# Optimization experiments

Hardware: AMD Instinct MI355X
Metric: run time of the kernel (lower is better)

The kernel has to match this reference:

```python
import jax, jax.numpy as jnp
import numpy as np

B, S, IN, OUT = 4, 2048, 4096, 11008


def setup_inputs() -> dict:
    key = jax.random.key(0)
    k1, k2, k3, k4 = jax.random.split(key, 4)
    x = jax.random.normal(k1, (B, S, IN), dtype=jnp.float32)
    # int8 weight codes (stored as int32 for portability; values in [0,127))
    weight_int8 = jax.random.randint(k2, (OUT, IN), 0, 127, dtype=jnp.int32)
    scale = jax.random.uniform(k3, (OUT,), dtype=jnp.float32) * 0.01 + 1e-4
    bias = jax.random.normal(k4, (OUT,), dtype=jnp.float32)
    return {"x": x, "weight_int8": weight_int8, "scale": scale, "bias": bias}


def reference(x, weight_int8, scale, bias):
    # dequantize: int8 codes -> fp, per-output-row scale (scale.view(-1,1) in torch)
    w = weight_int8.astype(jnp.float32) * scale[:, None]  # [OUT, IN]
    # F.linear(x, w, bias) == x @ w.T + bias
    out = jnp.einsum('bsi,oi->bso', x, w) + bias  # [B, S, OUT]
    return out
```

## Files before the change

kernel.cpp:

```cpp
#include <hip/hip_runtime.h>
#include <hip/hip_bf16.h>
#include <stdint.h>


#define MT 8192
#define KT 4096
#define NT 11008
#define NKT 32
#define MTILES 32
#define NTILES 43
#define CHUNK_BYTES 32768

typedef __attribute__((ext_vector_type(8))) short short8;
typedef __attribute__((ext_vector_type(4))) float f32x4;
typedef __attribute__((ext_vector_type(4))) int i32x4;
typedef __attribute__((ext_vector_type(16))) char char16;

static __device__ __forceinline__ short f2bf(float f) {
  union { float f; unsigned u; } c; c.f = f;
  unsigned u = c.u;
  return (short)((u + 0x7fffu + ((u >> 16) & 1u)) >> 16);
}

__global__ __launch_bounds__(256) void quant_x_kernel(const float* __restrict__ in,
                                                      char* __restrict__ Aws,
                                                      float* __restrict__ sx) {
  const int m = blockIdx.x;
  const int t = threadIdx.x;
  const float* row = in + (size_t)m * KT + t * 16;
  f32x4 v[4];
  float mx = 0.f;
#pragma unroll
  for (int i = 0; i < 4; i++) {
    v[i] = *(const f32x4*)(row + i * 4);
#pragma unroll
    for (int j = 0; j < 4; j++) mx = fmaxf(mx, fabsf(v[i][j]));
  }
#pragma unroll
  for (int off = 32; off; off >>= 1) mx = fmaxf(mx, __shfl_xor(mx, off));
  __shared__ float smx[4];
  if ((t & 63) == 0) smx[t >> 6] = mx;
  __syncthreads();
  mx = fmaxf(fmaxf(smx[0], smx[1]), fmaxf(smx[2], smx[3]));
  const float inv = 127.0f / mx;
  if (t == 0) sx[m] = mx * (1.0f / 127.0f);
  char16 q;
#pragma unroll
  for (int i = 0; i < 4; i++)
#pragma unroll
    for (int j = 0; j < 4; j++) q[i * 4 + j] = (char)(int)rintf(v[i][j] * inv);
  const int mt = m >> 8, r = m & 255, kt = t >> 3, g = t & 7;
  *(char16*)(Aws + ((size_t)mt * NKT + kt) * CHUNK_BYTES + r * 128 +
             ((g * 16) ^ ((r & 7) << 4))) = q;
}

__global__ __launch_bounds__(256) void cvt_w8_kernel(const int* __restrict__ in,
                                                     char* __restrict__ Bws) {
  const int n = blockIdx.x;
  const int t = threadIdx.x;
  const int* s = in + (size_t)n * KT + t * 16;
  char16 q;
#pragma unroll
  for (int i = 0; i < 4; i++) {
    i32x4 a = *(const i32x4*)(s + i * 4);
#pragma unroll
    for (int j = 0; j < 4; j++) q[i * 4 + j] = (char)a[j];
  }
  const int nt = n >> 8, r = n & 255, kt = t >> 3, g = t & 7;
  *(char16*)(Bws + ((size_t)nt * NKT + kt) * CHUNK_BYTES + r * 128 +
             ((g * 16) ^ ((r & 7) << 4))) = q;
}


#define GLD(chunk, j, ldsbase)                                                   \
  __builtin_amdgcn_global_load_lds(                                              \
      (const __attribute__((address_space(1))) void*)((chunk) + (j) * 8192 +     \
                                                      tid * 16),                 \
      (__attribute__((address_space(3))) void*)((ldsbase) + (j) * 8192 +         \
                                                wid * 1024),                     \
      16, 0, 0)

#define BAR asm volatile("s_barrier" ::: "memory")
#define VMC6 asm volatile("s_waitcnt vmcnt(6)" ::: "memory")
#define VMC0 asm volatile("s_waitcnt vmcnt(0)" ::: "memory")
#define LGK8 asm volatile("s_waitcnt lgkmcnt(8)" ::: "memory")

#define LDAQ(q)                                                   \
  do {                                                            \
    const char* a_ = LA + (wr * 128 + (q) * 32) * 128 + laneoff;  \
    afr[0][0] = *(const i32x4*)(a_ + kbx0);                       \
    afr[0][1] = *(const i32x4*)(a_ + (kbx0 ^ 64));                \
    afr[1][0] = *(const i32x4*)(a_ + 2048 + kbx0);                \
    afr[1][1] = *(const i32x4*)(a_ + 2048 + (kbx0 ^ 64));         \
  } while (0)

#define MMQ(q)                                                                 \
  do {                                                                         \
    __builtin_amdgcn_s_setprio(1);                                             \
    _Pragma("unroll") for (int mi2 = 0; mi2 < 2; mi2++)                        \
        _Pragma("unroll") for (int ni = 0; ni < 4; ni++) {                     \
      acc[(q) * 2 + mi2][ni] = __builtin_amdgcn_mfma_i32_16x16x64_i8(          \
          afr[mi2][0], bfr[ni][0], acc[(q) * 2 + mi2][ni], 0, 0, 0);           \
      acc[(q) * 2 + mi2][ni] = __builtin_amdgcn_mfma_i32_16x16x64_i8(          \
          afr[mi2][1], bfr[ni][1], acc[(q) * 2 + mi2][ni], 0, 0, 0);           \
    }                                                                          \
    __builtin_amdgcn_s_setprio(0);                                             \
  } while (0)

__global__ __launch_bounds__(512, 2) void gemm256(
    const char* __restrict__ Aws, const char* __restrict__ Bws,
    const float* __restrict__ sx, const float* __restrict__ scale,
    const float* __restrict__ bias, float* __restrict__ out) {
  extern __shared__ char Lsm[];
  const int tid = threadIdx.x;
  const int lane = tid & 63;
  const int wid = tid >> 6;
  const int wr = wid >> 2;
  const int wc = wid & 3;

  const int bid = blockIdx.x;
  const int lid = (bid & 7) * 172 + (bid >> 3);
  const int g8 = lid / 344;
  const int r8 = lid - g8 * 344;
  const int mt = g8 * 8 + (r8 & 7);
  const int nt = r8 >> 3;

  const char* Ach = Aws + (size_t)mt * NKT * CHUNK_BYTES;
  const char* Bch = Bws + (size_t)nt * NKT * CHUNK_BYTES;

  const int laneoff = (lane & 15) * 128;
  const int kbx0 = ((lane >> 4) * 16) ^ ((lane & 7) << 4);

  i32x4 acc[8][4] = {{{0, 0, 0, 0}}};
  i32x4 bfr[4][2];
  i32x4 afr[2][2];

  {
    char* lA0 = Lsm;
    char* lB0 = Lsm + 32768;
    GLD(Bch, 0, lB0); GLD(Bch, 1, lB0); GLD(Bch, 2, lB0); GLD(Bch, 3, lB0);
    GLD(Ach, 0, lA0); GLD(Ach, 1, lA0); GLD(Ach, 2, lA0); GLD(Ach, 3, lA0);
    const char* A1 = Ach + CHUNK_BYTES;
    const char* B1 = Bch + CHUNK_BYTES;
    char* lA1 = Lsm + 65536;
    char* lB1 = Lsm + 65536 + 32768;
    GLD(B1, 0, lB1); GLD(B1, 1, lB1); GLD(B1, 2, lB1); GLD(B1, 3, lB1);
    GLD(A1, 0, lA1); GLD(A1, 2, lA1);
    VMC6;
    BAR;
  }

  for (int t = 0; t < NKT; ++t) {
    const int c = t & 1;
    char* LA = Lsm + c * 65536;
    char* LB = LA + 32768;
    char* LAn = Lsm + (c ^ 1) * 65536;
    const char* C1A = Ach + CHUNK_BYTES;
    const char* C2A = Ach + 2 * CHUNK_BYTES;
    const char* C2B = Bch + 2 * CHUNK_BYTES;
    const bool st1 = (t + 1 < NKT);
    const bool st2 = (t + 2 < NKT);

    {
      const char* b_ = LB + wc * 8192 + laneoff;
#pragma unroll
      for (int ni = 0; ni < 4; ni++) {
        bfr[ni][0] = *(const i32x4*)(b_ + ni * 2048 + kbx0);
        bfr[ni][1] = *(const i32x4*)(b_ + ni * 2048 + (kbx0 ^ 64));
      }
      LDAQ(0);
      if (st1) { GLD(C1A, 1, LAn); GLD(C1A, 3, LAn); }
      LGK8;
      BAR;
      MMQ(0);
      BAR;
    }
    {
      LDAQ(1);
      if (st2) { GLD(C2B, 0, LB); GLD(C2B, 1, LB); }
      BAR;
      MMQ(1);
      BAR;
    }
    {
      LDAQ(2);
      if (st2) { GLD(C2B, 2, LB); GLD(C2B, 3, LB); }
      BAR;
      MMQ(2);
      BAR;
    }
    {
      LDAQ(3);
      if (st2) { GLD(C2A, 0, LA); GLD(C2A, 2, LA); }
      BAR;
      MMQ(3);
      if (st2) { VMC6; } else { VMC0; }
      BAR;
    }
    Ach += CHUNK_BYTES;
    Bch += CHUNK_BYTES;
  }

  const int col0 = nt * 256 + wc * 64 + (lane & 15);
  const int row0 = mt * 256 + wr * 128 + ((lane >> 4) << 2);
  float sxv[8][4];
#pragma unroll
  for (int mi = 0; mi < 8; mi++)
#pragma unroll
    for (int j = 0; j < 4; j++) sxv[mi][j] = sx[row0 + mi * 16 + j];
#pragma unroll
  for (int ni = 0; ni < 4; ni++) {
    const int n = col0 + ni * 16;
    const float sc = scale[n];
    const float bs = bias[n];
#pragma unroll
    for (int mi = 0; mi < 8; mi++) {
      const size_t base = (size_t)(row0 + mi * 16) * NT + n;
#pragma unroll
      for (int j = 0; j < 4; j++)
        out[base + (size_t)j * NT] = (float)acc[mi][ni][j] * (sxv[mi][j] * sc) + bs;
    }
  }
}

__global__ __launch_bounds__(256) void gemm_fallback(
    const float* __restrict__ Ap, const int* __restrict__ Bp,
    const float* __restrict__ scale, const float* __restrict__ bias,
    float* __restrict__ out) {
  __shared__ short ldsA[128 * 64];
  __shared__ short ldsB[128 * 64];
  const int tid = threadIdx.x;
  const int lane = tid & 63;
  const int wid = tid >> 6;
  const int nbn = NT / 128;
  const int cpx = ((MT / 128) * nbn) / 8;
  const int bid = blockIdx.x;
  const int wg = (bid & 7) * cpx + (bid >> 3);
  const int brow = (wg / nbn) * 128;
  const int bcol = (wg % nbn) * 128;
  const int wr = wid >> 1, wc = wid & 1;
  f32x4 acc[4][4] = {{{0.f, 0.f, 0.f, 0.f}}};
  const int srow = tid >> 3;
  const int sk8 = (tid & 7) * 8;
  for (int k0 = 0; k0 < KT; k0 += 64) {
    __syncthreads();
#pragma unroll
    for (int p = 0; p < 4; p++) {
      const int row = p * 32 + srow;
      const float* s = Ap + (size_t)(brow + row) * KT + k0 + sk8;
      f32x4 lo = *(const f32x4*)s;
      f32x4 hi = *(const f32x4*)(s + 4);
      short8 v;
#pragma unroll
      for (int j = 0; j < 4; j++) { v[j] = f2bf(lo[j]); v[4 + j] = f2bf(hi[j]); }
      int bo = (row * 64 + sk8) * 2;
      bo ^= ((row & 7) << 4);
      *(short8*)((char*)ldsA + bo) = v;
    }
#pragma unroll
    for (int p = 0; p < 4; p++) {
      const int row = p * 32 + srow;
      const int* s = Bp + (size_t)(bcol + row) * KT + k0 + sk8;
      i32x4 lo = *(const i32x4*)s;
      i32x4 hi = *(const i32x4*)(s + 4);
      short8 v;
#pragma unroll
      for (int j = 0; j < 4; j++) { v[j] = f2bf((float)lo[j]); v[4 + j] = f2bf((float)hi[j]); }
      int bo = (row * 64 + sk8) * 2;
      bo ^= ((row & 7) << 4);
      *(short8*)((char*)ldsB + bo) = v;
    }
    __syncthreads();
#pragma unroll
    for (int kk = 0; kk < 2; kk++) {
      short8 af[4], bf2[4];
#pragma unroll
      for (int mi = 0; mi < 4; mi++) {
        const int row = wr * 64 + mi * 16 + (lane & 15);
        int bo = (row * 64 + kk * 32 + (lane >> 4) * 8) * 2;
        bo ^= ((row & 7) << 4);
        af[mi] = *(const short8*)((const char*)ldsA + bo);
      }
#pragma unroll
      for (int ni = 0; ni < 4; ni++) {
        const int row = wc * 64 + ni * 16 + (lane & 15);
        int bo = (row * 64 + kk * 32 + (lane >> 4) * 8) * 2;
        bo ^= ((row & 7) << 4);
        bf2[ni] = *(const short8*)((const char*)ldsB + bo);
      }
#pragma unroll
      for (int mi = 0; mi < 4; mi++)
#pragma unroll
        for (int ni = 0; ni < 4; ni++)
          acc[mi][ni] = __builtin_amdgcn_mfma_f32_16x16x32_bf16(af[mi], bf2[ni],
                                                                acc[mi][ni], 0, 0, 0);
    }
  }
#pragma unroll
  for (int ni = 0; ni < 4; ni++) {
    const int n = bcol + wc * 64 + ni * 16 + (lane & 15);
    const float sc = scale[n];
    const float bs = bias[n];
#pragma unroll
    for (int mi = 0; mi < 4; mi++) {
      const int m0 = brow + wr * 64 + mi * 16 + ((lane >> 4) << 2);
#pragma unroll
      for (int j = 0; j < 4; j++)
        out[(size_t)(m0 + j) * NT + n] = acc[mi][ni][j] * sc + bs;
    }
  }
}

extern "C" void kernel_launch(void* const* d_in, const int* in_sizes, int n_in,
                              void* d_out, int out_size, void* d_ws, size_t ws_size,
                              hipStream_t stream) {
  const float* x = (const float*)d_in[0];
  const int* w = (const int*)d_in[1];
  const float* scale = (const float*)d_in[2];
  const float* bias = (const float*)d_in[3];
  float* out = (float*)d_out;

  const size_t a_bytes = (size_t)MTILES * NKT * CHUNK_BYTES;
  const size_t b_bytes = (size_t)NTILES * NKT * CHUNK_BYTES;
  const size_t s_bytes = (size_t)MT * sizeof(float);

  if (ws_size >= a_bytes + b_bytes + s_bytes) {
    char* aw = (char*)d_ws;
    char* bw = aw + a_bytes;
    float* sx = (float*)(bw + b_bytes);
    quant_x_kernel<<<dim3(MT), dim3(256), 0, stream>>>(x, aw, sx);
    cvt_w8_kernel<<<dim3(NT), dim3(256), 0, stream>>>(w, bw);
    hipFuncSetAttribute((const void*)gemm256,
                        hipFuncAttributeMaxDynamicSharedMemorySize, 131072);
    gemm256<<<dim3(MTILES * NTILES), dim3(512), 131072, stream>>>(
        aw, bw, sx, scale, bias, out);
  } else {
    gemm_fallback<<<dim3((MT / 128) * (NT / 128)), dim3(256), 0, stream>>>(
        x, w, scale, bias, out);
  }
}
```

Measured before the change: 476.3 us.

## Switch int8 GEMM to 32x32x32 MFMA with register double-buffered LDS fragments

```diff
diff --git a/kernel.cpp b/kernel.cpp
--- a/kernel.cpp
+++ b/kernel.cpp
@@ -14,6 +14,7 @@
 typedef __attribute__((ext_vector_type(8))) short short8;
 typedef __attribute__((ext_vector_type(4))) float f32x4;
 typedef __attribute__((ext_vector_type(4))) int i32x4;
+typedef __attribute__((ext_vector_type(16))) int i32x16;
 typedef __attribute__((ext_vector_type(16))) char char16;
 
 static __device__ __forceinline__ short f2bf(float f) {
@@ -81,29 +82,29 @@
       16, 0, 0)
 
 #define BAR asm volatile("s_barrier" ::: "memory")
-#define VMC6 asm volatile("s_waitcnt vmcnt(6)" ::: "memory")
 #define VMC0 asm volatile("s_waitcnt vmcnt(0)" ::: "memory")
-#define LGK8 asm volatile("s_waitcnt lgkmcnt(8)" ::: "memory")
-
-#define LDAQ(q)                                                   \
-  do {                                                            \
-    const char* a_ = LA + (wr * 128 + (q) * 32) * 128 + laneoff;  \
-    afr[0][0] = *(const i32x4*)(a_ + kbx0);                       \
-    afr[0][1] = *(const i32x4*)(a_ + (kbx0 ^ 64));                \
-    afr[1][0] = *(const i32x4*)(a_ + 2048 + kbx0);                \
-    afr[1][1] = *(const i32x4*)(a_ + 2048 + (kbx0 ^ 64));         \
+#define LGK0 asm volatile("s_waitcnt lgkmcnt(0)" ::: "memory")
+
+#define KOFF(s) ((((s) * 32) + khalf) ^ swz)
+
+#define LDSL(LAp, s, aset, bset)                                \
+  do {                                                          \
+    const int ko_ = KOFF(s);                                    \
+    aset[0] = *(const i32x4*)((LAp) + aoff + ko_);              \
+    aset[1] = *(const i32x4*)((LAp) + aoff + 4096 + ko_);       \
+    aset[2] = *(const i32x4*)((LAp) + aoff + 8192 + ko_);       \
+    aset[3] = *(const i32x4*)((LAp) + aoff + 12288 + ko_);      \
+    bset[0] = *(const i32x4*)((LAp) + boff + ko_);              \
+    bset[1] = *(const i32x4*)((LAp) + boff + 4096 + ko_);       \
   } while (0)
 
-#define MMQ(q)                                                                 \
+#define MMS(aset, bset)                                                        \
   do {                                                                         \
     __builtin_amdgcn_s_setprio(1);                                             \
-    _Pragma("unroll") for (int mi2 = 0; mi2 < 2; mi2++)                        \
-        _Pragma("unroll") for (int ni = 0; ni < 4; ni++) {                     \
-      acc[(q) * 2 + mi2][ni] = __builtin_amdgcn_mfma_i32_16x16x64_i8(          \
-          afr[mi2][0], bfr[ni][0], acc[(q) * 2 + mi2][ni], 0, 0, 0);           \
-      acc[(q) * 2 + mi2][ni] = __builtin_amdgcn_mfma_i32_16x16x64_i8(          \
-          afr[mi2][1], bfr[ni][1], acc[(q) * 2 + mi2][ni], 0, 0, 0);           \
-    }                                                                          \
+    _Pragma("unroll") for (int mb = 0; mb < 4; mb++)                           \
+        _Pragma("unroll") for (int nb = 0; nb < 2; nb++)                       \
+            acc[mb][nb] = __builtin_amdgcn_mfma_i32_32x32x32_i8(               \
+                aset[mb], bset[nb], acc[mb][nb], 0, 0, 0);                     \
     __builtin_amdgcn_s_setprio(0);                                             \
   } while (0)
 
@@ -128,97 +129,79 @@
   const char* Ach = Aws + (size_t)mt * NKT * CHUNK_BYTES;
   const char* Bch = Bws + (size_t)nt * NKT * CHUNK_BYTES;
 
-  const int laneoff = (lane & 15) * 128;
-  const int kbx0 = ((lane >> 4) * 16) ^ ((lane & 7) << 4);
-
-  i32x4 acc[8][4] = {{{0, 0, 0, 0}}};
-  i32x4 bfr[4][2];
-  i32x4 afr[2][2];
+  const int aoff = (wr * 128 + (lane & 31)) * 128;
+  const int boff = 32768 + (wc * 64 + (lane & 31)) * 128;
+  const int khalf = (lane >> 5) * 16;
+  const int swz = (lane & 7) << 4;
+
+  i32x16 acc[4][2] = {};
+  i32x4 a0[4], a1[4], b0[2], b1[2];
 
   {
     char* lA0 = Lsm;
     char* lB0 = Lsm + 32768;
     GLD(Bch, 0, lB0); GLD(Bch, 1, lB0); GLD(Bch, 2, lB0); GLD(Bch, 3, lB0);
     GLD(Ach, 0, lA0); GLD(Ach, 1, lA0); GLD(Ach, 2, lA0); GLD(Ach, 3, lA0);
+    VMC0;
+    BAR;
     const char* A1 = Ach + CHUNK_BYTES;
     const char* B1 = Bch + CHUNK_BYTES;
     char* lA1 = Lsm + 65536;
     char* lB1 = Lsm + 65536 + 32768;
     GLD(B1, 0, lB1); GLD(B1, 1, lB1); GLD(B1, 2, lB1); GLD(B1, 3, lB1);
-    GLD(A1, 0, lA1); GLD(A1, 2, lA1);
-    VMC6;
+    GLD(A1, 0, lA1); GLD(A1, 1, lA1); GLD(A1, 2, lA1); GLD(A1, 3, lA1);
+    LDSL(Lsm, 0, a0, b0);
+  }
+
+  for (int t = 0; t < NKT; ++t) {
+    const char* LA = Lsm + (t & 1) * 65536;
+
+    LDSL(LA, 1, a1, b1);  MMS(a0, b0);
+    LDSL(LA, 2, a0, b0);  MMS(a1, b1);
+    LDSL(LA, 3, a1, b1);  MMS(a0, b0);
+    MMS(a1, b1);
+
+    LGK0;
+    VMC0;
     BAR;
-  }
-
-  for (int t = 0; t < NKT; ++t) {
-    const int c = t & 1;
-    char* LA = Lsm + c * 65536;
-    char* LB = LA + 32768;
-    char* LAn = Lsm + (c ^ 1) * 65536;
-    const char* C1A = Ach + CHUNK_BYTES;
-    const char* C2A = Ach + 2 * CHUNK_BYTES;
-    const char* C2B = Bch + 2 * CHUNK_BYTES;
-    const bool st1 = (t + 1 < NKT);
-    const bool st2 = (t + 2 < NKT);
-
-    {
-      const char* b_ = LB + wc * 8192 + laneoff;
-#pragma unroll
-      for (int ni = 0; ni < 4; ni++) {
-        bfr[ni][0] = *(const i32x4*)(b_ + ni * 2048 + kbx0);
-        bfr[ni][1] = *(const i32x4*)(b_ + ni * 2048 + (kbx0 ^ 64));
+
+    if (t + 1 < NKT) {
+      const char* LAn = Lsm + ((t + 1) & 1) * 65536;
+      if (t + 2 < NKT) {
+        char* dA = Lsm + (t & 1) * 65536;
+        char* dB = dA + 32768;
+        const char* A2 = Ach + 2 * CHUNK_BYTES;
+        const char* B2 = Bch + 2 * CHUNK_BYTES;
+        GLD(B2, 0, dB); GLD(B2, 1, dB); GLD(B2, 2, dB); GLD(B2, 3, dB);
+        GLD(A2, 0, dA); GLD(A2, 1, dA); GLD(A2, 2, dA); GLD(A2, 3, dA);
       }
-      LDAQ(0);
-      if (st1) { GLD(C1A, 1, LAn); GLD(C1A, 3, LAn); }
-      LGK8;
-      BAR;
-      MMQ(0);
-      BAR;
-    }
-    {
-      LDAQ(1);
-      if (st2) { GLD(C2B, 0, LB); GLD(C2B, 1, LB); }
-      BAR;
-      MMQ(1);
-      BAR;
-    }
-    {
-      LDAQ(2);
-      if (st2) { GLD(C2B, 2, LB); GLD(C2B, 3, LB); }
-      BAR;
-      MMQ(2);
-      BAR;
-    }
-    {
-      LDAQ(3);
-      if (st2) { GLD(C2A, 0, LA); GLD(C2A, 2, LA); }
-      BAR;
-      MMQ(3);
-      if (st2) { VMC6; } else { VMC0; }
-      BAR;
+      LDSL(LAn, 0, a0, b0);
     }
     Ach += CHUNK_BYTES;
     Bch += CHUNK_BYTES;
   }
 
-  const int col0 = nt * 256 + wc * 64 + (lane & 15);
-  const int row0 = mt * 256 + wr * 128 + ((lane >> 4) << 2);
-  float sxv[8][4];
-#pragma unroll
-  for (int mi = 0; mi < 8; mi++)
-#pragma unroll
-    for (int j = 0; j < 4; j++) sxv[mi][j] = sx[row0 + mi * 16 + j];
-#pragma unroll
-  for (int ni = 0; ni < 4; ni++) {
-    const int n = col0 + ni * 16;
-    const float sc = scale[n];
-    const float bs = bias[n];
-#pragma unroll
-    for (int mi = 0; mi < 8; mi++) {
-      const size_t base = (size_t)(row0 + mi * 16) * NT + n;
-#pragma unroll
-      for (int j = 0; j < 4; j++)
-        out[base + (size_t)j * NT] = (float)acc[mi][ni][j] * (sxv[mi][j] * sc) + bs;
+  const int col0 = nt * 256 + wc * 64 + (lane & 31);
+  const int row0 = mt * 256 + wr * 128 + ((lane >> 5) << 2);
+#pragma unroll
+  for (int mb = 0; mb < 4; mb++) {
+    f32x4 sxq[4];
+#pragma unroll
+    for (int g = 0; g < 4; g++)
+      sxq[g] = *(const f32x4*)(sx + row0 + mb * 32 + g * 8);
+#pragma unroll
+    for (int nb = 0; nb < 2; nb++) {
+      const int n = col0 + nb * 32;
+      const float sc = scale[n];
+      const float bs = bias[n];
+#pragma unroll
+      for (int g = 0; g < 4; g++)
+#pragma unroll
+        for (int j = 0; j < 4; j++) {
+          const int row = row0 + mb * 32 + g * 8 + j;
+          out[(size_t)row * NT + n] =
+              (float)acc[mb][nb][g * 4 + j] * (sxq[g][j] * sc) + bs;
+        }
     }
   }
 }
```

Result: no change. 483.0 us (+1.4%).
